# Optimization experiments

Measured on AMD Instinct MI355X. Metric: run time of the kernel, lower is better.

## Reference

```python
import jax, jax.numpy as jnp
import numpy as np


def setup_inputs() -> dict:
    key = jax.random.key(0)
    ks = jax.random.split(key, 9)
    B, S, D, DK, DV = 4, 4096, 1024, 128, 128
    scale = 1.0 / np.sqrt(D)
    return {
        "q": jax.random.normal(ks[0], (B, S, D), jnp.float32),
        "k": jax.random.normal(ks[1], (B, S, D), jnp.float32),
        "v": jax.random.normal(ks[2], (B, S, D), jnp.float32),
        "Wq": jax.random.normal(ks[3], (D, DK), jnp.float32) * scale,
        "bq": jnp.zeros((DK,), jnp.float32),
        "Wk": jax.random.normal(ks[4], (D, DK), jnp.float32) * scale,
        "bk": jnp.zeros((DK,), jnp.float32),
        "Wv": jax.random.normal(ks[5], (D, DV), jnp.float32) * scale,
        "bv": jnp.zeros((DV,), jnp.float32),
    }


def reference(q, k, v, Wq, bq, Wk, bk, Wv, bv):
    # Q/K/V projections (nn.Linear)
    Q = q @ Wq + bq          # [B,S,DK]
    K = k @ Wk + bk          # [B,S,DK]
    V = v @ Wv + bv          # [B,S,DV]
    scale = Q.shape[-1] ** 0.5
    scores = jnp.einsum("bqd,bkd->bqk", Q, K) / scale  # [B,Sq,Sk]
    attn = jax.nn.softmax(scores, axis=-1)
    return jnp.einsum("bqk,bkd->bqd", attn, V)          # [B,Sq,DV]
```

## Files before the change

kernel.cpp:

```cpp
#include <hip/hip_runtime.h>
#include <hip/hip_bf16.h>
#include <cstdint>
#include <cmath>


typedef __bf16 bf16x8 __attribute__((ext_vector_type(8)));
typedef float f32x4 __attribute__((ext_vector_type(4)));
typedef float f32x16 __attribute__((ext_vector_type(16)));

typedef const __attribute__((address_space(1))) unsigned int* gp_t;
typedef __attribute__((address_space(3))) unsigned int* lp_t;

__device__ __forceinline__ unsigned short f2bf(float f) {
  unsigned u = __float_as_uint(f);
  u += 0x7fffu + ((u >> 16) & 1u);
  return (unsigned short)(u >> 16);
}

__device__ __forceinline__ bf16x8 ld_frag(const char* p) {
  uint4 u = *reinterpret_cast<const uint4*>(p);
  return __builtin_bit_cast(bf16x8, u);
}

__device__ __forceinline__ unsigned cvtpk_bf16(float lo, float hi) {
  unsigned r;
  asm("v_cvt_pk_bf16_f32 %0, %1, %2" : "=v"(r) : "v"(lo), "v"(hi));
  return r;
}

__device__ __forceinline__ void pl32swap(unsigned &a, unsigned &b) {
  asm("v_permlane32_swap_b32 %0, %1" : "+v"(a), "+v"(b));
}

__device__ __forceinline__ bf16x8 mk_frag(unsigned w0, unsigned w1, unsigned w2, unsigned w3) {
  uint4 u{w0, w1, w2, w3};
  return __builtin_bit_cast(bf16x8, u);
}

__device__ __forceinline__ bf16x8 cvt_frag(const float4& f0, const float4& f1) {
  return mk_frag(cvtpk_bf16(f0.x, f0.y), cvtpk_bf16(f0.z, f0.w),
                 cvtpk_bf16(f1.x, f1.y), cvtpk_bf16(f1.z, f1.w));
}

#define QSCALE_LOG2E 0.12751744f

__global__ __launch_bounds__(256) void prep_wt_kernel(
    const float* __restrict__ W0, const float* __restrict__ W1, const float* __restrict__ W2,
    unsigned short* __restrict__ T0, unsigned short* __restrict__ T1,
    unsigned short* __restrict__ T2) {
  const int mode = blockIdx.z;
  const float* W = (mode == 0) ? W0 : (mode == 1) ? W1 : W2;
  unsigned short* Wt = (mode == 0) ? T0 : (mode == 1) ? T1 : T2;
  __shared__ float tile[64][65];
  int kt = blockIdx.x, nt = blockIdx.y;
  int tid = threadIdx.x;
  int c = tid & 63;
  int r0 = (tid >> 6) * 16;
#pragma unroll
  for (int i = 0; i < 16; ++i) {
    int r = r0 + i;
    tile[r][c] = W[(size_t)(kt * 64 + r) * 128 + nt * 64 + c];
  }
  __syncthreads();
#pragma unroll
  for (int i = 0; i < 16; ++i) {
    int n = r0 + i;
    Wt[(size_t)(nt * 64 + n) * 1024 + kt * 64 + c] = f2bf(tile[c][n]);
  }
}

__global__ __launch_bounds__(512, 4) void proj_kernel(
    const float* __restrict__ qx, const float* __restrict__ kx, const float* __restrict__ vx,
    const unsigned short* __restrict__ Wtq, const unsigned short* __restrict__ Wtk,
    const unsigned short* __restrict__ Wtv,
    const float* __restrict__ bq, const float* __restrict__ bk, const float* __restrict__ bv,
    unsigned short* __restrict__ Qb, unsigned short* __restrict__ Kb,
    unsigned short* __restrict__ Vtb) {
  const int mode = blockIdx.y;
  const float* x = (mode == 0) ? qx : (mode == 1) ? kx : vx;
  const unsigned short* Wt = (mode == 0) ? Wtq : (mode == 1) ? Wtk : Wtv;
  const float* bias = (mode == 0) ? bq : (mode == 1) ? bk : bv;

  __shared__ __align__(16) char ldsW[49152];

  const int tid = threadIdx.x;
  const int lane = tid & 63, wid = tid >> 6;
  const int l15 = lane & 15, hi = lane >> 4;
  const long row0 = (long)blockIdx.x * 128;

  const float* a_base = x + (row0 + wid * 16 + l15) * 1024 + hi * 8;
  const char* w_src = (const char*)Wt + (size_t)(tid >> 3) * 2048 +
                      (size_t)((tid & 7) ^ ((tid >> 3) & 7)) * 16;

  f32x4 acc[8];
#pragma unroll
  for (int i = 0; i < 8; ++i) acc[i] = f32x4{0.f, 0.f, 0.f, 0.f};

  float4 aA[4], aB[4];

#define PROJ_STAGE_W(TS)                                                              \
  {                                                                                   \
    char* lw_ = ldsW + ((TS) % 3) * 16384;                                            \
    _Pragma("unroll")                                                                 \
    for (int i = 0; i < 2; ++i)                                                       \
      __builtin_amdgcn_global_load_lds((gp_t)(w_src + (size_t)i * 131072 + (TS) * 128),\
                                       (lp_t)(lw_ + i * 8192 + wid * 1024), 16, 0, 0);\
  }

#pragma unroll
  for (int kk = 0; kk < 2; ++kk)
#pragma unroll
    for (int h = 0; h < 2; ++h)
      aA[kk * 2 + h] = *reinterpret_cast<const float4*>(a_base + kk * 32 + h * 4);
  PROJ_STAGE_W(0);
  PROJ_STAGE_W(1);

#define PROJ_ITER(T, CUR, NXT)                                                        \
  {                                                                                   \
    if ((T) < 15) asm volatile("s_waitcnt vmcnt(2)" ::: "memory");                    \
    else          asm volatile("s_waitcnt vmcnt(0)" ::: "memory");                    \
    __builtin_amdgcn_s_barrier();                                                     \
    __builtin_amdgcn_sched_barrier(0);                                                \
    if ((T) < 15) {                                                                   \
      _Pragma("unroll")                                                               \
      for (int kk = 0; kk < 2; ++kk)                                                  \
        _Pragma("unroll")                                                             \
        for (int h = 0; h < 2; ++h)                                                   \
          NXT[kk * 2 + h] = *reinterpret_cast<const float4*>(                         \
              a_base + ((T) + 1) * 64 + kk * 32 + h * 4);                             \
    }                                                                                 \
    if ((T) < 14) PROJ_STAGE_W((T) + 2);                                              \
    bf16x8 af0 = cvt_frag(CUR[0], CUR[1]);                                            \
    bf16x8 af1 = cvt_frag(CUR[2], CUR[3]);                                            \
    char* lwc_ = ldsW + ((T) % 3) * 16384;                                            \
    __builtin_amdgcn_s_setprio(1);                                                    \
    _Pragma("unroll")                                                                 \
    for (int ni = 0; ni < 8; ++ni) {                                                  \
      int row = ni * 16 + l15;                                                        \
      int swz = (row & 7) << 4;                                                       \
      bf16x8 wf0 = ld_frag(lwc_ + ((row * 128 + hi * 16) ^ swz));                     \
      bf16x8 wf1 = ld_frag(lwc_ + ((row * 128 + 64 + hi * 16) ^ swz));                \
      acc[ni] = __builtin_amdgcn_mfma_f32_16x16x32_bf16(af0, wf0, acc[ni], 0, 0, 0);  \
      acc[ni] = __builtin_amdgcn_mfma_f32_16x16x32_bf16(af1, wf1, acc[ni], 0, 0, 0);  \
    }                                                                                 \
    __builtin_amdgcn_s_setprio(0);                                                    \
  }

#pragma unroll
  for (int t = 0; t < 16; ++t) {
    if (t & 1) PROJ_ITER(t, aB, aA)
    else       PROJ_ITER(t, aA, aB)
  }

#undef PROJ_ITER
#undef PROJ_STAGE_W

#pragma unroll
  for (int ni = 0; ni < 8; ++ni) {
    int n = ni * 16 + l15;
    float bv_ = bias[n];
    long m = row0 + wid * 16 + hi * 4;
    f32x4 a = acc[ni];
    if (mode == 2) {
      int bb = (int)(m >> 12);
      int s = (int)(m & 4095);
      ushort4 pk;
      pk.x = f2bf(a.x + bv_); pk.y = f2bf(a.y + bv_);
      pk.z = f2bf(a.z + bv_); pk.w = f2bf(a.w + bv_);
      *reinterpret_cast<ushort4*>(Vtb + ((size_t)(bb * 128 + n)) * 4096 + s) = pk;
    } else {
      const float sc = (mode == 0) ? QSCALE_LOG2E : 1.0f;
      unsigned short* outp = (mode == 0) ? Qb : Kb;
      outp[(m + 0) * 128 + n] = f2bf((a.x + bv_) * sc);
      outp[(m + 1) * 128 + n] = f2bf((a.y + bv_) * sc);
      outp[(m + 2) * 128 + n] = f2bf((a.z + bv_) * sc);
      outp[(m + 3) * 128 + n] = f2bf((a.w + bv_) * sc);
    }
  }
}

template <int TPS>
__global__ __launch_bounds__(256, 2) void attn_kernel(
    const unsigned short* __restrict__ Qb, const unsigned short* __restrict__ Kb,
    const unsigned short* __restrict__ Vtb, float* __restrict__ Po,
    float* __restrict__ ml) {
  __shared__ __align__(16) char lds[65536];

  const int tid = threadIdx.x;
  const int lane = tid & 63, wid = tid >> 6;
  const int l31 = lane & 31, hi = lane >> 5;
  const int split = blockIdx.y;
  const int b = blockIdx.z;
  const int qbase = blockIdx.x * 128 + wid * 32;
  const size_t growq = (size_t)b * 4096 + qbase + l31;

  const char* kg0 = (const char*)Kb + (size_t)(b * 4096) * 256;
  const char* vg0 = (const char*)Vtb + (size_t)b * 128 * 4096 * 2;
  const int k_row = tid >> 4;
  const int k_csw = (tid & 15) ^ (k_row & 7);
  const int v_dv = tid >> 3;
  const int v_csw = (tid & 7) ^ (v_dv & 7);

#define ATTN_STAGE(KV0, BUF)                                                          \
  {                                                                                   \
    char* kb_ = lds + (BUF) * 16384;                                                  \
    char* vb_ = lds + 32768 + (BUF) * 16384;                                          \
    const char* kgs_ = kg0 + (size_t)(KV0) * 256 + (size_t)k_row * 256 + k_csw * 16;  \
    const char* vgs_ = vg0 + (size_t)(KV0) * 2 + (size_t)v_dv * 8192 + v_csw * 16;    \
    _Pragma("unroll")                                                                 \
    for (int i = 0; i < 4; ++i)                                                       \
      __builtin_amdgcn_global_load_lds((gp_t)(kgs_ + (size_t)i * 4096),               \
                                       (lp_t)(kb_ + i * 4096 + wid * 1024), 16, 0, 0);\
    _Pragma("unroll")                                                                 \
    for (int i = 0; i < 4; ++i)                                                       \
      __builtin_amdgcn_global_load_lds((gp_t)(vgs_ + (size_t)i * 262144),             \
                                       (lp_t)(vb_ + i * 4096 + wid * 1024), 16, 0, 0);\
  }

  bf16x8 qf[8];
  {
    const unsigned short* qp = Qb + growq * 128 + hi * 8;
#pragma unroll
    for (int kt = 0; kt < 8; ++kt)
      qf[kt] = __builtin_bit_cast(bf16x8, *reinterpret_cast<const uint4*>(qp + kt * 16));
  }

  f32x16 oacc[4];
#pragma unroll
  for (int d = 0; d < 4; ++d)
#pragma unroll
    for (int j = 0; j < 16; ++j) oacc[d][j] = 0.f;
  float mrun = -INFINITY, lrun = 0.f;

  const int t0 = split * TPS, t1 = t0 + TPS;

  ATTN_STAGE(t0 * 64, 0);
  ATTN_STAGE((t0 + 1) * 64, 1);

#pragma unroll 1
  for (int t = t0; t < t1; ++t) {
    const int buf = (t - t0) & 1;
    if (t < t1 - 1) asm volatile("s_waitcnt vmcnt(8)" ::: "memory");
    else            asm volatile("s_waitcnt vmcnt(0)" ::: "memory");
    __builtin_amdgcn_s_barrier();
    __builtin_amdgcn_sched_barrier(0);
    char* ldsK = lds + buf * 16384;
    char* ldsV = lds + 32768 + buf * 16384;

    f32x16 sc0, sc1;
#pragma unroll
    for (int j = 0; j < 16; ++j) { sc0[j] = 0.f; sc1[j] = 0.f; }
    __builtin_amdgcn_s_setprio(1);
#pragma unroll
    for (int kvb = 0; kvb < 2; ++kvb) {
      int row = kvb * 32 + l31;
      int rowoff = row * 256, swz = (row & 7) << 4;
#pragma unroll
      for (int kt = 0; kt < 8; ++kt) {
        bf16x8 kf = ld_frag(ldsK + ((rowoff + kt * 32 + hi * 16) ^ swz));
        if (kvb == 0) sc0 = __builtin_amdgcn_mfma_f32_32x32x16_bf16(kf, qf[kt], sc0, 0, 0, 0);
        else          sc1 = __builtin_amdgcn_mfma_f32_32x32x16_bf16(kf, qf[kt], sc1, 0, 0, 0);
      }
    }
    __builtin_amdgcn_s_setprio(0);

    float tmx[16];
#pragma unroll
    for (int i = 0; i < 16; ++i) tmx[i] = fmaxf(sc0[i], sc1[i]);
#pragma unroll
    for (int s = 8; s > 0; s >>= 1)
#pragma unroll
      for (int i = 0; i < s; ++i) tmx[i] = fmaxf(tmx[i], tmx[i + s]);
    float mt = tmx[0];
    mt = fmaxf(mt, __shfl_xor(mt, 32));

    if (!__all(mt - mrun <= 8.0f)) {
      float mnew = fmaxf(mrun, mt);
      float scl = exp2f(mrun - mnew);
      mrun = mnew;
      lrun *= scl;
#pragma unroll
      for (int d = 0; d < 4; ++d)
#pragma unroll
        for (int j = 0; j < 16; ++j) oacc[d][j] *= scl;
    }

#pragma unroll
    for (int i = 0; i < 16; ++i) {
      sc0[i] = exp2f(sc0[i] - mrun);
      sc1[i] = exp2f(sc1[i] - mrun);
    }
    float ts[16];
#pragma unroll
    for (int i = 0; i < 16; ++i) ts[i] = sc0[i] + sc1[i];
#pragma unroll
    for (int s = 8; s > 0; s >>= 1)
#pragma unroll
      for (int i = 0; i < s; ++i) ts[i] += ts[i + s];
    float psum = ts[0];
    psum += __shfl_xor(psum, 32);
    lrun += psum;

    bf16x8 pa[4];
#pragma unroll
    for (int c = 0; c < 2; ++c) {
      const f32x16& p = c ? sc1 : sc0;
#pragma unroll
      for (int g = 0; g < 2; ++g) {
        const int base = g * 8;
        unsigned a0 = cvtpk_bf16(p[base + 0], p[base + 1]);
        unsigned b0 = cvtpk_bf16(p[base + 4], p[base + 5]);
        pl32swap(a0, b0);
        unsigned a1 = cvtpk_bf16(p[base + 2], p[base + 3]);
        unsigned b1 = cvtpk_bf16(p[base + 6], p[base + 7]);
        pl32swap(a1, b1);
        pa[c * 2 + g] = mk_frag(a0, a1, b0, b1);
      }
    }

    __builtin_amdgcn_s_setprio(1);
#pragma unroll
    for (int dvb = 0; dvb < 4; ++dvb) {
      int vrow = dvb * 32 + l31;
      int voff = vrow * 128, vswz = (vrow & 7) << 4;
#pragma unroll
      for (int tt = 0; tt < 4; ++tt) {
        bf16x8 vf = ld_frag(ldsV + ((voff + tt * 32 + hi * 16) ^ vswz));
        oacc[dvb] = __builtin_amdgcn_mfma_f32_32x32x16_bf16(vf, pa[tt], oacc[dvb], 0, 0, 0);
      }
    }
    __builtin_amdgcn_s_setprio(0);

    __builtin_amdgcn_s_barrier();
    __builtin_amdgcn_sched_barrier(0);
    if (t + 2 < t1) ATTN_STAGE((t + 2) * 64, buf);
  }

#undef ATTN_STAGE

  if (hi == 0) {
    float* mlp = ml + (size_t)split * 32768 + growq * 2;
    mlp[0] = mrun; mlp[1] = lrun;
  }

  float* po = Po + ((size_t)split << 21) + ((size_t)b * 4096 + qbase) * 128;
  char* tbase = lds + wid * 4096;
  for (int dvb = 0; dvb < 4; ++dvb) {
#pragma unroll
    for (int g = 0; g < 4; ++g) {
      float4 w4{oacc[dvb][g * 4 + 0], oacc[dvb][g * 4 + 1],
                oacc[dvb][g * 4 + 2], oacc[dvb][g * 4 + 3]};
      int off = (l31 * 128 + g * 32 + hi * 16) ^ ((l31 & 7) << 4);
      *reinterpret_cast<float4*>(tbase + off) = w4;
    }
    asm volatile("s_waitcnt lgkmcnt(0)" ::: "memory");
    __builtin_amdgcn_sched_barrier(0);
#pragma unroll
    for (int qq = 0; qq < 4; ++qq) {
      int q = qq * 8 + (lane >> 3);
      int off = (q * 128 + (lane & 7) * 16) ^ ((q & 7) << 4);
      float4 r4 = *reinterpret_cast<const float4*>(tbase + off);
      *reinterpret_cast<float4*>(po + (size_t)q * 128 + dvb * 32 + (lane & 7) * 4) = r4;
    }
    asm volatile("s_waitcnt lgkmcnt(0)" ::: "memory");
    __builtin_amdgcn_sched_barrier(0);
  }
}

template <int NS>
__global__ __launch_bounds__(256) void combine_kernel(const float* __restrict__ Po,
                                                      const float* __restrict__ ml,
                                                      float* __restrict__ out) {
  int idx = blockIdx.x * 256 + threadIdx.x;
  int grow = idx >> 5;
  int c4 = (idx & 31) * 4;
  float m[NS], l[NS];
  float M = -INFINITY;
#pragma unroll
  for (int s = 0; s < NS; ++s) {
    m[s] = ml[(size_t)s * 32768 + grow * 2 + 0];
    l[s] = ml[(size_t)s * 32768 + grow * 2 + 1];
    M = fmaxf(M, m[s]);
  }
  float L = 0.f, w[NS];
#pragma unroll
  for (int s = 0; s < NS; ++s) {
    w[s] = exp2f(m[s] - M);
    L += l[s] * w[s];
  }
  float invL = 1.0f / L;
  float4 acc = {0.f, 0.f, 0.f, 0.f};
#pragma unroll
  for (int s = 0; s < NS; ++s) {
    float4 p = *reinterpret_cast<const float4*>(Po + ((size_t)s << 21) + (size_t)grow * 128 + c4);
    acc.x += p.x * w[s]; acc.y += p.y * w[s];
    acc.z += p.z * w[s]; acc.w += p.w * w[s];
  }
  acc.x *= invL; acc.y *= invL; acc.z *= invL; acc.w *= invL;
  *reinterpret_cast<float4*>(out + (size_t)grow * 128 + c4) = acc;
}

extern "C" void kernel_launch(void* const* d_in, const int* in_sizes, int n_in,
                              void* d_out, int out_size, void* d_ws, size_t ws_size,
                              hipStream_t stream) {
  const float* q  = (const float*)d_in[0];
  const float* k  = (const float*)d_in[1];
  const float* v  = (const float*)d_in[2];
  const float* Wq = (const float*)d_in[3];
  const float* bq = (const float*)d_in[4];
  const float* Wk = (const float*)d_in[5];
  const float* bk = (const float*)d_in[6];
  const float* Wv = (const float*)d_in[7];
  const float* bv = (const float*)d_in[8];
  float* out = (float*)d_out;

  char* ws = (char*)d_ws;
  unsigned short* Qb  = (unsigned short*)(ws);
  unsigned short* Kb  = (unsigned short*)(ws + (4u << 20));
  unsigned short* Vtb = (unsigned short*)(ws + (8u << 20));
  unsigned short* Wtq = (unsigned short*)(ws + (12u << 20));
  unsigned short* Wtk = (unsigned short*)(ws + (12u << 20) + (256u << 10));
  unsigned short* Wtv = (unsigned short*)(ws + (12u << 20) + (512u << 10));

  const size_t base = (size_t)13 << 20;
  const size_t per = ((size_t)8 << 20) + ((size_t)128 << 10);
  int nsplit = 1;
  if (ws_size >= base + 4 * per) nsplit = 4;
  else if (ws_size >= base + 2 * per) nsplit = 2;
  float* Po = (float*)(ws + base);
  float* ml = (float*)(ws + base + (size_t)nsplit * ((size_t)8 << 20));

  prep_wt_kernel<<<dim3(16, 2, 3), 256, 0, stream>>>(Wq, Wk, Wv, Wtq, Wtk, Wtv);
  proj_kernel<<<dim3(128, 3), 512, 0, stream>>>(q, k, v, Wtq, Wtk, Wtv, bq, bk, bv, Qb, Kb, Vtb);
  if (nsplit == 4) {
    attn_kernel<16><<<dim3(32, 4, 4), 256, 0, stream>>>(Qb, Kb, Vtb, Po, ml);
    combine_kernel<4><<<2048, 256, 0, stream>>>(Po, ml, out);
  } else if (nsplit == 2) {
    attn_kernel<32><<<dim3(32, 2, 4), 256, 0, stream>>>(Qb, Kb, Vtb, Po, ml);
    combine_kernel<2><<<2048, 256, 0, stream>>>(Po, ml, out);
  } else {
    attn_kernel<64><<<dim3(32, 1, 4), 256, 0, stream>>>(Qb, Kb, Vtb, Po, ml);
    combine_kernel<1><<<2048, 256, 0, stream>>>(Po, ml, out);
  }
}
```

Baseline: 103.6 us.

## Halve projection block size and deepen A-operand prefetch to three stages

The projection kernel now uses 256-thread blocks covering 64 rows each, doubling the grid to 256x3 blocks so more CUs get work. Each block still stages the full weight tile, so each thread issues four global_load_lds calls per stage instead of two. The activation loads are triple-buffered with a two-stage-ahead prefetch, and vmcnt waits are tuned to keep more loads in flight. A second barrier per iteration guards LDS buffer reuse, which adds sync overhead, and weight traffic per output row doubles.

```diff
diff --git a/kernel.cpp b/kernel.cpp
--- a/kernel.cpp
+++ b/kernel.cpp
@@ -69,7 +69,7 @@
   }
 }
 
-__global__ __launch_bounds__(512, 4) void proj_kernel(
+__global__ __launch_bounds__(256, 3) void proj_kernel(
     const float* __restrict__ qx, const float* __restrict__ kx, const float* __restrict__ vx,
     const unsigned short* __restrict__ Wtq, const unsigned short* __restrict__ Wtk,
     const unsigned short* __restrict__ Wtv,
@@ -86,9 +86,10 @@
   const int tid = threadIdx.x;
   const int lane = tid & 63, wid = tid >> 6;
   const int l15 = lane & 15, hi = lane >> 4;
-  const long row0 = (long)blockIdx.x * 128;
+  const long row0 = (long)blockIdx.x * 64;
 
   const float* a_base = x + (row0 + wid * 16 + l15) * 1024 + hi * 8;
+
   const char* w_src = (const char*)Wt + (size_t)(tid >> 3) * 2048 +
                       (size_t)((tid & 7) ^ ((tid >> 3) & 7)) * 16;
 
@@ -96,42 +97,41 @@
 #pragma unroll
   for (int i = 0; i < 8; ++i) acc[i] = f32x4{0.f, 0.f, 0.f, 0.f};
 
-  float4 aA[4], aB[4];
-
-#define PROJ_STAGE_W(TS)                                                              \
+  float4 aA[4], aB[4], aC[4];
+
+#define PROJ_A_ISSUE(TS, SET)                                                         \
+  {                                                                                   \
+    const float* an_ = a_base + (TS) * 64;                                            \
+    SET[0] = *reinterpret_cast<const float4*>(an_ + 0);                               \
+    SET[1] = *reinterpret_cast<const float4*>(an_ + 4);                               \
+    SET[2] = *reinterpret_cast<const float4*>(an_ + 32);                              \
+    SET[3] = *reinterpret_cast<const float4*>(an_ + 36);                              \
+  }
+
+#define PROJ_W_ISSUE(TS)                                                              \
   {                                                                                   \
     char* lw_ = ldsW + ((TS) % 3) * 16384;                                            \
     _Pragma("unroll")                                                                 \
-    for (int i = 0; i < 2; ++i)                                                       \
-      __builtin_amdgcn_global_load_lds((gp_t)(w_src + (size_t)i * 131072 + (TS) * 128),\
-                                       (lp_t)(lw_ + i * 8192 + wid * 1024), 16, 0, 0);\
-  }
-
-#pragma unroll
-  for (int kk = 0; kk < 2; ++kk)
-#pragma unroll
-    for (int h = 0; h < 2; ++h)
-      aA[kk * 2 + h] = *reinterpret_cast<const float4*>(a_base + kk * 32 + h * 4);
-  PROJ_STAGE_W(0);
-  PROJ_STAGE_W(1);
-
-#define PROJ_ITER(T, CUR, NXT)                                                        \
+    for (int i = 0; i < 4; ++i)                                                       \
+      __builtin_amdgcn_global_load_lds((gp_t)(w_src + (size_t)i * 65536 + (TS) * 128),\
+                                       (lp_t)(lw_ + i * 4096 + wid * 1024), 16, 0, 0);\
+  }
+
+  PROJ_A_ISSUE(0, aA);
+  PROJ_W_ISSUE(0);
+  PROJ_A_ISSUE(1, aB);
+  PROJ_W_ISSUE(1);
+  PROJ_A_ISSUE(2, aC);
+
+#define PROJ_ITER(T, SET, VM)                                                         \
   {                                                                                   \
-    if ((T) < 15) asm volatile("s_waitcnt vmcnt(2)" ::: "memory");                    \
-    else          asm volatile("s_waitcnt vmcnt(0)" ::: "memory");                    \
+    if ((T) + 2 <= 15) PROJ_W_ISSUE((T) + 2);                                         \
+    asm volatile("s_waitcnt vmcnt(" #VM ")" ::: "memory");                            \
     __builtin_amdgcn_s_barrier();                                                     \
     __builtin_amdgcn_sched_barrier(0);                                                \
-    if ((T) < 15) {                                                                   \
-      _Pragma("unroll")                                                               \
-      for (int kk = 0; kk < 2; ++kk)                                                  \
-        _Pragma("unroll")                                                             \
-        for (int h = 0; h < 2; ++h)                                                   \
-          NXT[kk * 2 + h] = *reinterpret_cast<const float4*>(                         \
-              a_base + ((T) + 1) * 64 + kk * 32 + h * 4);                             \
-    }                                                                                 \
-    if ((T) < 14) PROJ_STAGE_W((T) + 2);                                              \
-    bf16x8 af0 = cvt_frag(CUR[0], CUR[1]);                                            \
-    bf16x8 af1 = cvt_frag(CUR[2], CUR[3]);                                            \
+    bf16x8 af0 = cvt_frag(SET[0], SET[1]);                                            \
+    bf16x8 af1 = cvt_frag(SET[2], SET[3]);                                            \
+    if ((T) + 3 <= 15) PROJ_A_ISSUE((T) + 3, SET);                                    \
     char* lwc_ = ldsW + ((T) % 3) * 16384;                                            \
     __builtin_amdgcn_s_setprio(1);                                                    \
     _Pragma("unroll")                                                                 \
@@ -144,16 +144,20 @@
       acc[ni] = __builtin_amdgcn_mfma_f32_16x16x32_bf16(af1, wf1, acc[ni], 0, 0, 0);  \
     }                                                                                 \
     __builtin_amdgcn_s_setprio(0);                                                    \
-  }
-
-#pragma unroll
-  for (int t = 0; t < 16; ++t) {
-    if (t & 1) PROJ_ITER(t, aB, aA)
-    else       PROJ_ITER(t, aA, aB)
-  }
+    __builtin_amdgcn_s_barrier();                                                     \
+    __builtin_amdgcn_sched_barrier(0);                                                \
+  }
+
+  PROJ_ITER(0, aA, 16)  PROJ_ITER(1, aB, 16)  PROJ_ITER(2, aC, 16)
+  PROJ_ITER(3, aA, 16)  PROJ_ITER(4, aB, 16)  PROJ_ITER(5, aC, 16)
+  PROJ_ITER(6, aA, 16)  PROJ_ITER(7, aB, 16)  PROJ_ITER(8, aC, 16)
+  PROJ_ITER(9, aA, 16)  PROJ_ITER(10, aB, 16) PROJ_ITER(11, aC, 16)
+  PROJ_ITER(12, aA, 16) PROJ_ITER(13, aB, 16) PROJ_ITER(14, aC, 8)
+  PROJ_ITER(15, aA, 0)
 
 #undef PROJ_ITER
-#undef PROJ_STAGE_W
+#undef PROJ_W_ISSUE
+#undef PROJ_A_ISSUE
 
 #pragma unroll
   for (int ni = 0; ni < 8; ++ni) {
@@ -431,7 +435,7 @@
   float* ml = (float*)(ws + base + (size_t)nsplit * ((size_t)8 << 20));
 
   prep_wt_kernel<<<dim3(16, 2, 3), 256, 0, stream>>>(Wq, Wk, Wv, Wtq, Wtk, Wtv);
-  proj_kernel<<<dim3(128, 3), 512, 0, stream>>>(q, k, v, Wtq, Wtk, Wtv, bq, bk, bv, Qb, Kb, Vtb);
+  proj_kernel<<<dim3(256, 3), 256, 0, stream>>>(q, k, v, Wtq, Wtk, Wtv, bq, bk, bv, Qb, Kb, Vtb);
   if (nsplit == 4) {
     attn_kernel<16><<<dim3(32, 4, 4), 256, 0, stream>>>(Qb, Kb, Vtb, Po, ml);
     combine_kernel<4><<<2048, 256, 0, stream>>>(Po, ml, out);
```

Result: no change. 103.3 us (-0.4%).

## Restructure projection GEMM to stage activations through LDS with smaller blocks

Applied to the files above, without the earlier changes.

The projection kernel now uses 64-row tiles with 256 threads and 768 blocks instead of 128-row tiles with 512 threads. Each K-step of 128 loads fp32 activations with coalesced row-wise reads, converts them to bf16 and writes them into swizzled LDS. The weights go to LDS through direct global-to-LDS loads. The old triple-buffered, register-prefetched pipeline is replaced by a simple single-buffered loop with two barriers per step. This trades latency hiding inside a block for more blocks and better-coalesced activation loads, so load latency is now exposed at each barrier.

```diff
diff --git a/kernel.cpp b/kernel.cpp
--- a/kernel.cpp
+++ b/kernel.cpp
@@ -35,11 +35,6 @@
 __device__ __forceinline__ bf16x8 mk_frag(unsigned w0, unsigned w1, unsigned w2, unsigned w3) {
   uint4 u{w0, w1, w2, w3};
   return __builtin_bit_cast(bf16x8, u);
-}
-
-__device__ __forceinline__ bf16x8 cvt_frag(const float4& f0, const float4& f1) {
-  return mk_frag(cvtpk_bf16(f0.x, f0.y), cvtpk_bf16(f0.z, f0.w),
-                 cvtpk_bf16(f1.x, f1.y), cvtpk_bf16(f1.z, f1.w));
 }
 
 #define QSCALE_LOG2E 0.12751744f
@@ -69,7 +64,7 @@
   }
 }
 
-__global__ __launch_bounds__(512, 4) void proj_kernel(
+__global__ __launch_bounds__(256, 3) void proj_kernel(
     const float* __restrict__ qx, const float* __restrict__ kx, const float* __restrict__ vx,
     const unsigned short* __restrict__ Wtq, const unsigned short* __restrict__ Wtk,
     const unsigned short* __restrict__ Wtv,
@@ -81,79 +76,66 @@
   const unsigned short* Wt = (mode == 0) ? Wtq : (mode == 1) ? Wtk : Wtv;
   const float* bias = (mode == 0) ? bq : (mode == 1) ? bk : bv;
 
-  __shared__ __align__(16) char ldsW[49152];
+  __shared__ __align__(16) char lds[49152];
+  char* ldsA = lds;
+  char* ldsW = lds + 16384;
 
   const int tid = threadIdx.x;
   const int lane = tid & 63, wid = tid >> 6;
   const int l15 = lane & 15, hi = lane >> 4;
-  const long row0 = (long)blockIdx.x * 128;
-
-  const float* a_base = x + (row0 + wid * 16 + l15) * 1024 + hi * 8;
-  const char* w_src = (const char*)Wt + (size_t)(tid >> 3) * 2048 +
-                      (size_t)((tid & 7) ^ ((tid >> 3) & 7)) * 16;
+  const long row0 = (long)blockIdx.x * 64;
+
+  const int a_row0 = tid >> 5;
+  const int a_c16  = tid & 31;
+  const float* a_src = x + (row0 + a_row0) * 1024 + a_c16 * 4;
+  const int a_swz = (a_row0 & 7) << 4;
+  const int a_wbyte = (((a_c16 >> 1) * 16) ^ a_swz) + (a_c16 & 1) * 8;
+
+  const char* w_src = (const char*)Wt + (size_t)(tid >> 4) * 2048 +
+                      (size_t)((tid & 15) ^ ((tid >> 4) & 7)) * 16;
 
   f32x4 acc[8];
 #pragma unroll
   for (int i = 0; i < 8; ++i) acc[i] = f32x4{0.f, 0.f, 0.f, 0.f};
 
-  float4 aA[4], aB[4];
-
-#define PROJ_STAGE_W(TS)                                                              \
-  {                                                                                   \
-    char* lw_ = ldsW + ((TS) % 3) * 16384;                                            \
-    _Pragma("unroll")                                                                 \
-    for (int i = 0; i < 2; ++i)                                                       \
-      __builtin_amdgcn_global_load_lds((gp_t)(w_src + (size_t)i * 131072 + (TS) * 128),\
-                                       (lp_t)(lw_ + i * 8192 + wid * 1024), 16, 0, 0);\
-  }
-
-#pragma unroll
-  for (int kk = 0; kk < 2; ++kk)
-#pragma unroll
-    for (int h = 0; h < 2; ++h)
-      aA[kk * 2 + h] = *reinterpret_cast<const float4*>(a_base + kk * 32 + h * 4);
-  PROJ_STAGE_W(0);
-  PROJ_STAGE_W(1);
-
-#define PROJ_ITER(T, CUR, NXT)                                                        \
-  {                                                                                   \
-    if ((T) < 15) asm volatile("s_waitcnt vmcnt(2)" ::: "memory");                    \
-    else          asm volatile("s_waitcnt vmcnt(0)" ::: "memory");                    \
-    __builtin_amdgcn_s_barrier();                                                     \
-    __builtin_amdgcn_sched_barrier(0);                                                \
-    if ((T) < 15) {                                                                   \
-      _Pragma("unroll")                                                               \
-      for (int kk = 0; kk < 2; ++kk)                                                  \
-        _Pragma("unroll")                                                             \
-        for (int h = 0; h < 2; ++h)                                                   \
-          NXT[kk * 2 + h] = *reinterpret_cast<const float4*>(                         \
-              a_base + ((T) + 1) * 64 + kk * 32 + h * 4);                             \
-    }                                                                                 \
-    if ((T) < 14) PROJ_STAGE_W((T) + 2);                                              \
-    bf16x8 af0 = cvt_frag(CUR[0], CUR[1]);                                            \
-    bf16x8 af1 = cvt_frag(CUR[2], CUR[3]);                                            \
-    char* lwc_ = ldsW + ((T) % 3) * 16384;                                            \
-    __builtin_amdgcn_s_setprio(1);                                                    \
-    _Pragma("unroll")                                                                 \
-    for (int ni = 0; ni < 8; ++ni) {                                                  \
-      int row = ni * 16 + l15;                                                        \
-      int swz = (row & 7) << 4;                                                       \
-      bf16x8 wf0 = ld_frag(lwc_ + ((row * 128 + hi * 16) ^ swz));                     \
-      bf16x8 wf1 = ld_frag(lwc_ + ((row * 128 + 64 + hi * 16) ^ swz));                \
-      acc[ni] = __builtin_amdgcn_mfma_f32_16x16x32_bf16(af0, wf0, acc[ni], 0, 0, 0);  \
-      acc[ni] = __builtin_amdgcn_mfma_f32_16x16x32_bf16(af1, wf1, acc[ni], 0, 0, 0);  \
-    }                                                                                 \
-    __builtin_amdgcn_s_setprio(0);                                                    \
-  }
-
-#pragma unroll
-  for (int t = 0; t < 16; ++t) {
-    if (t & 1) PROJ_ITER(t, aB, aA)
-    else       PROJ_ITER(t, aA, aB)
-  }
-
-#undef PROJ_ITER
-#undef PROJ_STAGE_W
+  const int arow = wid * 16 + l15;
+  const int aswzr = (arow & 7) << 4;
+
+#pragma unroll 1
+  for (int t = 0; t < 8; ++t) {
+    float4 av[8];
+#pragma unroll
+    for (int j = 0; j < 8; ++j)
+      av[j] = *reinterpret_cast<const float4*>(a_src + t * 128 + j * 8192);
+#pragma unroll
+    for (int i = 0; i < 8; ++i)
+      __builtin_amdgcn_global_load_lds((gp_t)(w_src + (size_t)i * 32768 + t * 256),
+                                       (lp_t)(ldsW + i * 4096 + wid * 1024), 16, 0, 0);
+#pragma unroll
+    for (int j = 0; j < 8; ++j) {
+      uint2 wv;
+      wv.x = cvtpk_bf16(av[j].x, av[j].y);
+      wv.y = cvtpk_bf16(av[j].z, av[j].w);
+      *reinterpret_cast<uint2*>(ldsA + a_row0 * 256 + j * 2048 + a_wbyte) = wv;
+    }
+    __syncthreads();
+
+    bf16x8 af[4];
+#pragma unroll
+    for (int kk = 0; kk < 4; ++kk)
+      af[kk] = ld_frag(ldsA + ((arow * 256 + (kk * 4 + hi) * 16) ^ aswzr));
+#pragma unroll
+    for (int ni = 0; ni < 8; ++ni) {
+      int n = ni * 16 + l15;
+      int nswz = (n & 7) << 4;
+#pragma unroll
+      for (int kk = 0; kk < 4; ++kk) {
+        bf16x8 wf = ld_frag(ldsW + ((n * 256 + (kk * 4 + hi) * 16) ^ nswz));
+        acc[ni] = __builtin_amdgcn_mfma_f32_16x16x32_bf16(af[kk], wf, acc[ni], 0, 0, 0);
+      }
+    }
+    __syncthreads();
+  }
 
 #pragma unroll
   for (int ni = 0; ni < 8; ++ni) {
@@ -431,7 +413,7 @@
   float* ml = (float*)(ws + base + (size_t)nsplit * ((size_t)8 << 20));
 
   prep_wt_kernel<<<dim3(16, 2, 3), 256, 0, stream>>>(Wq, Wk, Wv, Wtq, Wtk, Wtv);
-  proj_kernel<<<dim3(128, 3), 512, 0, stream>>>(q, k, v, Wtq, Wtk, Wtv, bq, bk, bv, Qb, Kb, Vtb);
+  proj_kernel<<<dim3(256, 3), 256, 0, stream>>>(q, k, v, Wtq, Wtk, Wtv, bq, bk, bv, Qb, Kb, Vtb);
   if (nsplit == 4) {
     attn_kernel<16><<<dim3(32, 4, 4), 256, 0, stream>>>(Qb, Kb, Vtb, Po, ml);
     combine_kernel<4><<<2048, 256, 0, stream>>>(Po, ml, out);
```

Result: no change. 103.7 us (+0.1%).
